# Kernel optimization log

Measured on AMD Instinct MI355X. Metric: run time of the kernel, lower is better.

Reference implementation:

```python
import jax, jax.numpy as jnp
import numpy as np

NUM_HEADS = 16
LN_EPS = 1e-5


def setup_inputs() -> dict:
    key = jax.random.key(0)
    k1, k2, k3 = jax.random.split(key, 3)
    E = 1024
    B, S = 4, 2048
    return {
        "rotation_params": jax.random.normal(k1, (E, E), dtype=jnp.float32) * (E ** -0.5),
        "entangle_params": jax.random.normal(k2, (E, E), dtype=jnp.float32) * (E ** -0.5),
        "inputs": jax.random.normal(k3, (B, S, E), dtype=jnp.float32),
        "ln_weight": jnp.ones((E,), dtype=jnp.float32),
        "ln_bias": jnp.zeros((E,), dtype=jnp.float32),
    }


def reference(rotation_params, entangle_params, inputs, ln_weight, ln_bias):
    x = inputs  # (B, S, E)
    B, S, E = x.shape
    H = NUM_HEADS
    D = E // H
    scale = D ** -0.5

    q = jnp.einsum('bse,ef->bsf', x, rotation_params)
    k = jnp.einsum('bse,ef->bsf', x, entangle_params)
    v = x  # forward uses raw inputs as values

    # split heads: (B, H, S, D)
    q = q.reshape(B, S, H, D).transpose(0, 2, 1, 3)
    k = k.reshape(B, S, H, D).transpose(0, 2, 1, 3)
    v = v.reshape(B, S, H, D).transpose(0, 2, 1, 3)

    scores = jnp.einsum('bhsd,bhtd->bhst', q, k) * scale  # (B, H, S, S)
    attn = jax.nn.softmax(scores, axis=-1)
    context = jnp.einsum('bhst,bhtd->bhsd', attn, v)
    context = context.transpose(0, 2, 1, 3).reshape(B, S, E)

    # residual + LayerNorm
    y = context + x
    mu = jnp.mean(y, axis=-1, keepdims=True)
    var = jnp.mean(jnp.square(y - mu), axis=-1, keepdims=True)
    y = (y - mu) * jax.lax.rsqrt(var + LN_EPS)
    return y * ln_weight + ln_bias
```

## Files before the change

kernel.cpp:

```cpp
#include <hip/hip_runtime.h>
#include <hip/hip_bf16.h>

#define LOG2E 1.44269504088896340736f

typedef __attribute__((ext_vector_type(8)))  short  short8;
typedef __attribute__((ext_vector_type(4)))  float  f32x4;
typedef __attribute__((ext_vector_type(16))) float  f32x16;

__device__ __forceinline__ unsigned short f2bf(float f) {
  unsigned u = __builtin_bit_cast(unsigned, f);
  return (unsigned short)((u + 0x8000u) >> 16);
}
__device__ __forceinline__ unsigned pkbf2(float a, float b) {
  unsigned A = __builtin_bit_cast(unsigned, a) + 0x8000u;
  unsigned B = __builtin_bit_cast(unsigned, b) + 0x8000u;
  return __builtin_amdgcn_perm(B, A, 0x07060302u);
}
__device__ __forceinline__ float hexp2(float x) {
  float r; asm("v_exp_f32 %0, %1" : "=v"(r) : "v"(x)); return r;
}
__device__ __forceinline__ void gl16(const void* g, void* l) {
  __builtin_amdgcn_global_load_lds(
      (const __attribute__((address_space(1))) void*)g,
      (__attribute__((address_space(3))) void*)l, 16, 0, 0);
}
__device__ __forceinline__ float vmax16(f32x16 s) {
  float a[8];
#pragma unroll
  for (int j = 0; j < 8; j++) a[j] = fmaxf(s[2 * j], s[2 * j + 1]);
#pragma unroll
  for (int j = 0; j < 4; j++) a[j] = fmaxf(a[j], a[j + 4]);
  return fmaxf(fmaxf(a[0], a[1]), fmaxf(a[2], a[3]));
}


__global__ __launch_bounds__(256) void prep_wt(const float* __restrict__ R,
                                               const float* __restrict__ En,
                                               unsigned short* __restrict__ Rt,
                                               unsigned short* __restrict__ Et) {
  const float* src = blockIdx.z ? En : R;
  unsigned short* dst = blockIdx.z ? Et : Rt;
  __shared__ unsigned short t[64][65];
  int e0 = blockIdx.y * 64, f0 = blockIdx.x * 64;
  int tid = threadIdx.x;
  int r = tid >> 2, c4 = (tid & 3) * 16;
#pragma unroll
  for (int j = 0; j < 16; j += 4) {
    float4 v = *(const float4*)(src + (size_t)(e0 + r) * 1024 + f0 + c4 + j);
    t[c4 + j + 0][r] = f2bf(v.x);
    t[c4 + j + 1][r] = f2bf(v.y);
    t[c4 + j + 2][r] = f2bf(v.z);
    t[c4 + j + 3][r] = f2bf(v.w);
  }
  __syncthreads();
  short8 o0, o1;
#pragma unroll
  for (int j = 0; j < 8; j++) {
    o0[j] = (short)t[r][c4 + j];
    o1[j] = (short)t[r][c4 + 8 + j];
  }
  *(short8*)(dst + (size_t)(f0 + r) * 1024 + e0 + c4) = o0;
  *(short8*)(dst + (size_t)(f0 + r) * 1024 + e0 + c4 + 8) = o1;
}

__global__ __launch_bounds__(256) void prep_vt(const float* __restrict__ x,
                                               unsigned short* __restrict__ vt,
                                               unsigned short* __restrict__ xb) {
  int bh = blockIdx.y, b = bh >> 4, h = bh & 15;
  int s0 = blockIdx.x * 64;
  __shared__ unsigned short t[64][65];
  int tid = threadIdx.x;
  int r = tid >> 2, c4 = (tid & 3) * 16;
#pragma unroll
  for (int j = 0; j < 16; j += 4) {
    float4 v = *(const float4*)(x + (size_t)(b * 2048 + s0 + r) * 1024 + h * 64 + c4 + j);
    ushort4 o;
    o.x = f2bf(v.x); o.y = f2bf(v.y); o.z = f2bf(v.z); o.w = f2bf(v.w);
    t[c4 + j + 0][r] = o.x;
    t[c4 + j + 1][r] = o.y;
    t[c4 + j + 2][r] = o.z;
    t[c4 + j + 3][r] = o.w;
    *(ushort4*)(xb + (size_t)(b * 2048 + s0 + r) * 1024 + h * 64 + c4 + j) = o;
  }
  __syncthreads();
  short8 o0, o1;
#pragma unroll
  for (int j = 0; j < 8; j++) {
    o0[j] = (short)t[r][c4 + j];
    o1[j] = (short)t[r][c4 + 8 + j];
  }
  *(short8*)(vt + (size_t)(bh * 64 + r) * 2048 + s0 + c4) = o0;
  *(short8*)(vt + (size_t)(bh * 64 + r) * 2048 + s0 + c4 + 8) = o1;
}

__global__ __launch_bounds__(256) void gemm_qk(const unsigned short* __restrict__ A,
                                               const unsigned short* __restrict__ Bw,
                                               unsigned short* __restrict__ out,
                                               float scale) {
  int m0 = blockIdx.x * 128, n0 = blockIdx.y * 128;
  int tid = threadIdx.x;
  int w = tid >> 6, l = tid & 63;
  int wr = w >> 1, wc = w & 1;
  int l15 = l & 15, lq = l >> 4;

  __shared__ unsigned short As[128 * 64];
  __shared__ unsigned short Bs[128 * 64];

  f32x4 acc[4][4] = {};

  for (int k0 = 0; k0 < 1024; k0 += 64) {
    __syncthreads();
#pragma unroll
    for (int i = 0; i < 4; i++) {
      int row = i * 32 + (tid >> 3), ch = tid & 7;
      gl16(A  + (size_t)(m0 + row) * 1024 + k0 + ((ch ^ (row & 7)) << 3),
           (char*)As + i * 4096 + w * 1024);
      gl16(Bw + (size_t)(n0 + row) * 1024 + k0 + ((ch ^ (row & 7)) << 3),
           (char*)Bs + i * 4096 + w * 1024);
    }
    __syncthreads();

    short8 af[4][2], bfr[4][2];
#pragma unroll
    for (int mf = 0; mf < 4; mf++)
#pragma unroll
      for (int kk = 0; kk < 2; kk++) {
        int row = wr * 64 + mf * 16 + l15;
        int kb2 = (kk * 32 + lq * 8) * 2;
        af[mf][kk] = *(const short8*)((const char*)As + row * 128 + (kb2 ^ ((row & 7) << 4)));
      }
#pragma unroll
    for (int nf = 0; nf < 4; nf++)
#pragma unroll
      for (int kk = 0; kk < 2; kk++) {
        int row = wc * 64 + nf * 16 + l15;
        int kb2 = (kk * 32 + lq * 8) * 2;
        bfr[nf][kk] = *(const short8*)((const char*)Bs + row * 128 + (kb2 ^ ((row & 7) << 4)));
      }
#pragma unroll
    for (int mf = 0; mf < 4; mf++)
#pragma unroll
      for (int nf = 0; nf < 4; nf++)
#pragma unroll
        for (int kk = 0; kk < 2; kk++)
          acc[mf][nf] = __builtin_amdgcn_mfma_f32_16x16x32_bf16(
              af[mf][kk], bfr[nf][kk], acc[mf][nf], 0, 0, 0);
  }

#pragma unroll
  for (int mf = 0; mf < 4; mf++)
#pragma unroll
    for (int nf = 0; nf < 4; nf++)
#pragma unroll
      for (int r = 0; r < 4; r++) {
        int grow = m0 + wr * 64 + mf * 16 + lq * 4 + r;
        int gcol = n0 + wc * 64 + nf * 16 + l15;
        out[(size_t)grow * 1024 + gcol] = f2bf(acc[mf][nf][r] * scale);
      }
}

__global__ __launch_bounds__(256) void attn_k(const unsigned short* __restrict__ Q,
                                              const unsigned short* __restrict__ K,
                                              const unsigned short* __restrict__ VT,
                                              float* __restrict__ ctx) {
  int f = blockIdx.x;
  int bh = ((f >> 7) << 3) | (f & 7);
  int qt = (f >> 3) & 15;
  int b = bh >> 4, h = bh & 15;
  int q0 = qt * 128;
  int tid = threadIdx.x;
  int w = tid >> 6, l = tid & 63;
  int lh = l >> 5, l31 = l & 31;

  __shared__ unsigned short Kl[2 * 64 * 64];
  __shared__ unsigned short Vl[2 * 64 * 64];

  int qrow = q0 + w * 32 + l31;
  const unsigned short* qp = Q + (size_t)(b * 2048 + qrow) * 1024 + h * 64;
  short8 qf[4];
#pragma unroll
  for (int dk = 0; dk < 4; dk++) qf[dk] = *(const short8*)(qp + dk * 16 + lh * 8);

  f32x16 cacc[2] = {};
  float mrun = -INFINITY, lsum = 0.f;

#define STAGE(buf, tt)                                                        \
  {                                                                           \
    _Pragma("unroll") for (int i_ = 0; i_ < 2; i_++) {                        \
      int row_ = i_ * 32 + (tid >> 3), ch_ = tid & 7;                         \
      gl16(K + (size_t)(b * 2048 + (tt) + row_) * 1024 + h * 64 +             \
               ((ch_ ^ (row_ & 7)) << 3),                                     \
           (char*)Kl + (buf) * 8192 + i_ * 4096 + w * 1024);                  \
      gl16(VT + (size_t)(bh * 64 + row_) * 2048 + (tt) +                      \
               ((ch_ ^ (row_ & 7)) << 3),                                     \
           (char*)Vl + (buf) * 8192 + i_ * 4096 + w * 1024);                  \
    }                                                                         \
  }

  STAGE(0, 0);
  __syncthreads();
  int cur = 0;

  for (int tc = 0; tc < 32; tc++) {
    int t0 = tc * 64;
    if (tc < 31) STAGE(cur ^ 1, t0 + 64);

    const char* Kb = (const char*)Kl + cur * 8192;
    const char* Vb = (const char*)Vl + cur * 8192;

    f32x16 sacc[2] = {};
    __builtin_amdgcn_s_setprio(1);
#pragma unroll
    for (int tf = 0; tf < 2; tf++) {
#pragma unroll
      for (int dk = 0; dk < 4; dk++) {
        int row = tf * 32 + l31;
        int kb2 = (dk * 16 + lh * 8) * 2;
        short8 kf = *(const short8*)(Kb + row * 128 + (kb2 ^ ((row & 7) << 4)));
        sacc[tf] = __builtin_amdgcn_mfma_f32_32x32x16_bf16(kf, qf[dk], sacc[tf], 0, 0, 0);
      }
    }
    __builtin_amdgcn_s_setprio(0);

    float tmax = fmaxf(vmax16(sacc[0]), vmax16(sacc[1]));
    {
      auto rr = __builtin_amdgcn_permlane32_swap(
          __builtin_bit_cast(unsigned, tmax), __builtin_bit_cast(unsigned, tmax), false, false);
      tmax = fmaxf(__builtin_bit_cast(float, rr[0]), __builtin_bit_cast(float, rr[1]));
    }

    if (!__all(tmax <= mrun + 8.f)) {
      float mnew = fmaxf(mrun, tmax);
      float alpha = hexp2(mrun - mnew);
      mrun = mnew;
      lsum *= alpha;
#pragma unroll
      for (int r = 0; r < 16; r++) {
        int rowq = (r & 3) + ((r >> 2) << 3) + (lh << 2);
        float ar = __shfl(alpha, rowq, 64);
        cacc[0][r] *= ar;
        cacc[1][r] *= ar;
      }
    }

    float racc0 = 0.f, racc1 = 0.f;
#pragma unroll
    for (int r = 0; r < 16; r++) {
      float p0 = hexp2(sacc[0][r] - mrun);
      float p1 = hexp2(sacc[1][r] - mrun);
      sacc[0][r] = p0;
      sacc[1][r] = p1;
      racc0 += p0;
      racc1 += p1;
    }
    float rs = racc0 + racc1;
    {
      auto rr = __builtin_amdgcn_permlane32_swap(
          __builtin_bit_cast(unsigned, rs), __builtin_bit_cast(unsigned, rs), false, false);
      rs = __builtin_bit_cast(float, rr[0]) + __builtin_bit_cast(float, rr[1]);
    }
    lsum += rs;

#pragma unroll
    for (int tf = 0; tf < 2; tf++) {
      short8 pa[2];
#pragma unroll
      for (int kk = 0; kk < 2; kk++) {
        int R = kk * 8;
        unsigned P0 = pkbf2(sacc[tf][R + 0], sacc[tf][R + 1]);
        unsigned P1 = pkbf2(sacc[tf][R + 2], sacc[tf][R + 3]);
        unsigned P2 = pkbf2(sacc[tf][R + 4], sacc[tf][R + 5]);
        unsigned P3 = pkbf2(sacc[tf][R + 6], sacc[tf][R + 7]);
        auto r02 = __builtin_amdgcn_permlane32_swap(P0, P2, false, false);
        auto r13 = __builtin_amdgcn_permlane32_swap(P1, P3, false, false);
        union { unsigned u[4]; short8 s8; } wv;
        wv.u[0] = r02[0];
        wv.u[1] = r13[0];
        wv.u[2] = r02[1];
        wv.u[3] = r13[1];
        pa[kk] = wv.s8;
      }
      __builtin_amdgcn_s_setprio(1);
#pragma unroll
      for (int kk = 0; kk < 2; kk++)
#pragma unroll
        for (int df = 0; df < 2; df++) {
          int drow = df * 32 + l31;
          int tb2 = (tf * 32 + kk * 16 + lh * 8) * 2;
          short8 vf = *(const short8*)(Vb + drow * 128 + (tb2 ^ ((l31 & 7) << 4)));
          cacc[df] = __builtin_amdgcn_mfma_f32_32x32x16_bf16(pa[kk], vf, cacc[df], 0, 0, 0);
        }
      __builtin_amdgcn_s_setprio(0);
    }

    __syncthreads();
    cur ^= 1;
  }
#undef STAGE

  float linv = 1.f / lsum;
#pragma unroll
  for (int r = 0; r < 16; r++) {
    int rowq = (r & 3) + ((r >> 2) << 3) + (lh << 2);
    float lr = __shfl(linv, rowq, 64);
    size_t base = (size_t)(b * 2048 + q0 + w * 32 + rowq) * 1024 + h * 64 + l31;
    ctx[base]      = cacc[0][r] * lr;
    ctx[base + 32] = cacc[1][r] * lr;
  }
}

__global__ __launch_bounds__(256) void ln_k(const float* __restrict__ ctx,
                                            const float* __restrict__ x,
                                            const float* __restrict__ wgt,
                                            const float* __restrict__ bgam,
                                            float* __restrict__ out) {
  int row = blockIdx.x;
  int tid = threadIdx.x;
  size_t base = (size_t)row * 1024 + tid * 4;
  float4 c = *(const float4*)(ctx + base);
  float4 xv = *(const float4*)(x + base);
  float4 y;
  y.x = c.x + xv.x; y.y = c.y + xv.y; y.z = c.z + xv.z; y.w = c.w + xv.w;
  float s  = y.x + y.y + y.z + y.w;
  float ss = y.x * y.x + y.y * y.y + y.z * y.z + y.w * y.w;
#pragma unroll
  for (int o = 32; o >= 1; o >>= 1) {
    s  += __shfl_xor(s, o, 64);
    ss += __shfl_xor(ss, o, 64);
  }
  __shared__ float sm[8];
  if ((tid & 63) == 0) { sm[(tid >> 6) * 2] = s; sm[(tid >> 6) * 2 + 1] = ss; }
  __syncthreads();
  s  = sm[0] + sm[2] + sm[4] + sm[6];
  ss = sm[1] + sm[3] + sm[5] + sm[7];
  float mu = s * (1.f / 1024.f);
  float var = ss * (1.f / 1024.f) - mu * mu;
  float rstd = rsqrtf(var + 1e-5f);
  float4 wv = *(const float4*)(wgt + tid * 4);
  float4 bv = *(const float4*)(bgam + tid * 4);
  float4 o4;
  o4.x = (y.x - mu) * rstd * wv.x + bv.x;
  o4.y = (y.y - mu) * rstd * wv.y + bv.y;
  o4.z = (y.z - mu) * rstd * wv.z + bv.z;
  o4.w = (y.w - mu) * rstd * wv.w + bv.w;
  *(float4*)(out + base) = o4;
}

extern "C" void kernel_launch(void* const* d_in, const int* in_sizes, int n_in,
                              void* d_out, int out_size, void* d_ws, size_t ws_size,
                              hipStream_t stream) {
  (void)in_sizes; (void)n_in; (void)out_size; (void)ws_size;
  const float* R  = (const float*)d_in[0];
  const float* En = (const float*)d_in[1];
  const float* x  = (const float*)d_in[2];
  const float* lw = (const float*)d_in[3];
  const float* lb = (const float*)d_in[4];
  float* out = (float*)d_out;

  char* ws = (char*)d_ws;
  unsigned short* xb  = (unsigned short*)(ws);
  unsigned short* qb  = (unsigned short*)(ws + (size_t)(16u << 20));
  unsigned short* kb  = (unsigned short*)(ws + (size_t)(32u << 20));
  unsigned short* vt  = (unsigned short*)(ws + (size_t)(48u << 20));
  float*          ctx = (float*)(ws + (size_t)(64u << 20));
  unsigned short* rt  = (unsigned short*)(ws + (size_t)(96u << 20));
  unsigned short* et  = (unsigned short*)(ws + (size_t)(98u << 20));

  prep_wt<<<dim3(16, 16, 2), 256, 0, stream>>>(R, En, rt, et);
  prep_vt<<<dim3(32, 64), 256, 0, stream>>>(x, vt, xb);
  gemm_qk<<<dim3(64, 8), 256, 0, stream>>>(xb, rt, qb, 0.125f * LOG2E);
  gemm_qk<<<dim3(64, 8), 256, 0, stream>>>(xb, et, kb, 1.0f);
  attn_k<<<1024, 256, 0, stream>>>(qb, kb, vt, ctx);
  ln_k<<<8192, 256, 0, stream>>>(ctx, x, lw, lb, out);
}
```

Measured before the change: 279.7 us.

## Fuse Q/K projections, unroll attention loop by two, store context in bf16

Merges the two projection GEMMs into one launch with a doubled N grid, relying on the transposed R and E weight buffers sitting next to each other in the workspace. The attention loop is unrolled by two with fixed LDS buffer offsets and precomputed swizzled addresses. Softmax now uses packed add and bf16 conversion instructions, and the row-sum cross-lane reduction moves out of the loop to run once at the end. The context is written as bf16 instead of fp32, halving the traffic between the attention and LayerNorm kernels at some precision cost, and launch bounds request higher occupancy.

```diff
diff --git a/kernel.cpp b/kernel.cpp
--- a/kernel.cpp
+++ b/kernel.cpp
@@ -4,6 +4,7 @@
 #define LOG2E 1.44269504088896340736f
 
 typedef __attribute__((ext_vector_type(8)))  short  short8;
+typedef __attribute__((ext_vector_type(2)))  float  f32x2;
 typedef __attribute__((ext_vector_type(4)))  float  f32x4;
 typedef __attribute__((ext_vector_type(16))) float  f32x16;
 
@@ -11,26 +12,25 @@
   unsigned u = __builtin_bit_cast(unsigned, f);
   return (unsigned short)((u + 0x8000u) >> 16);
 }
-__device__ __forceinline__ unsigned pkbf2(float a, float b) {
-  unsigned A = __builtin_bit_cast(unsigned, a) + 0x8000u;
-  unsigned B = __builtin_bit_cast(unsigned, b) + 0x8000u;
-  return __builtin_amdgcn_perm(B, A, 0x07060302u);
+__device__ __forceinline__ float bf2f(unsigned short u) {
+  return __builtin_bit_cast(float, (unsigned)u << 16);
+}
+__device__ __forceinline__ f32x2 pkadd(f32x2 a, f32x2 b) {
+  f32x2 r; asm("v_pk_add_f32 %0, %1, %2" : "=v"(r) : "v"(a), "v"(b)); return r;
+}
+__device__ __forceinline__ unsigned cvtpk2(float a, float b) {
+  unsigned r; asm("v_cvt_pk_bf16_f32 %0, %1, %2" : "=v"(r) : "v"(a), "v"(b)); return r;
 }
 __device__ __forceinline__ float hexp2(float x) {
   float r; asm("v_exp_f32 %0, %1" : "=v"(r) : "v"(x)); return r;
+}
+__device__ __forceinline__ float m3(float a, float b, float c) {
+  return fmaxf(fmaxf(a, b), c);
 }
 __device__ __forceinline__ void gl16(const void* g, void* l) {
   __builtin_amdgcn_global_load_lds(
       (const __attribute__((address_space(1))) void*)g,
       (__attribute__((address_space(3))) void*)l, 16, 0, 0);
-}
-__device__ __forceinline__ float vmax16(f32x16 s) {
-  float a[8];
-#pragma unroll
-  for (int j = 0; j < 8; j++) a[j] = fmaxf(s[2 * j], s[2 * j + 1]);
-#pragma unroll
-  for (int j = 0; j < 4; j++) a[j] = fmaxf(a[j], a[j + 4]);
-  return fmaxf(fmaxf(a[0], a[1]), fmaxf(a[2], a[3]));
 }
 
 
@@ -93,10 +93,11 @@
   *(short8*)(vt + (size_t)(bh * 64 + r) * 2048 + s0 + c4 + 8) = o1;
 }
 
-__global__ __launch_bounds__(256) void gemm_qk(const unsigned short* __restrict__ A,
-                                               const unsigned short* __restrict__ Bw,
-                                               unsigned short* __restrict__ out,
-                                               float scale) {
+__global__ __launch_bounds__(256) void gemm_qk2(const unsigned short* __restrict__ A,
+                                                const unsigned short* __restrict__ Bw,
+                                                unsigned short* __restrict__ qb,
+                                                unsigned short* __restrict__ kb,
+                                                float qs) {
   int m0 = blockIdx.x * 128, n0 = blockIdx.y * 128;
   int tid = threadIdx.x;
   int w = tid >> 6, l = tid & 63;
@@ -147,6 +148,9 @@
               af[mf][kk], bfr[nf][kk], acc[mf][nf], 0, 0, 0);
   }
 
+  unsigned short* out = (n0 < 1024) ? qb : kb;
+  float scale = (n0 < 1024) ? qs : 1.0f;
+  int cb = n0 & 1023;
 #pragma unroll
   for (int mf = 0; mf < 4; mf++)
 #pragma unroll
@@ -154,15 +158,15 @@
 #pragma unroll
       for (int r = 0; r < 4; r++) {
         int grow = m0 + wr * 64 + mf * 16 + lq * 4 + r;
-        int gcol = n0 + wc * 64 + nf * 16 + l15;
+        int gcol = cb + wc * 64 + nf * 16 + l15;
         out[(size_t)grow * 1024 + gcol] = f2bf(acc[mf][nf][r] * scale);
       }
 }
 
-__global__ __launch_bounds__(256) void attn_k(const unsigned short* __restrict__ Q,
-                                              const unsigned short* __restrict__ K,
-                                              const unsigned short* __restrict__ VT,
-                                              float* __restrict__ ctx) {
+__global__ __launch_bounds__(256, 4) void attn_k(const unsigned short* __restrict__ Q,
+                                                 const unsigned short* __restrict__ K,
+                                                 const unsigned short* __restrict__ VT,
+                                                 unsigned short* __restrict__ ctx) {
   int f = blockIdx.x;
   int bh = ((f >> 7) << 3) | (f & 7);
   int qt = (f >> 3) & 15;
@@ -181,8 +185,21 @@
 #pragma unroll
   for (int dk = 0; dk < 4; dk++) qf[dk] = *(const short8*)(qp + dk * 16 + lh * 8);
 
+  int key = (l31 & 7) << 4;
+  int koff[4], voff[4];
+#pragma unroll
+  for (int dk = 0; dk < 4; dk++) koff[dk] = l31 * 128 + ((dk * 32 + lh * 16) ^ key);
+#pragma unroll
+  for (int tf = 0; tf < 2; tf++)
+#pragma unroll
+    for (int kk = 0; kk < 2; kk++)
+      voff[tf * 2 + kk] = l31 * 128 + ((tf * 64 + kk * 32 + lh * 16) ^ key);
+
+  const char* KB = (const char*)Kl;
+  const char* VB = (const char*)Vl;
+
   f32x16 cacc[2] = {};
-  float mrun = -INFINITY, lsum = 0.f;
+  float mrun = -INFINITY, lsl = 0.f;
 
 #define STAGE(buf, tt)                                                        \
   {                                                                           \
@@ -197,119 +214,107 @@
     }                                                                         \
   }
 
+#define COMPUTE(IMM)                                                          \
+  do {                                                                        \
+    f32x16 sacc[2] = {};                                                      \
+    __builtin_amdgcn_s_setprio(1);                                            \
+    _Pragma("unroll") for (int tf = 0; tf < 2; tf++)                          \
+      _Pragma("unroll") for (int dk = 0; dk < 4; dk++) {                      \
+        short8 kf = *(const short8*)(KB + koff[dk] + (IMM) + tf * 4096);      \
+        sacc[tf] = __builtin_amdgcn_mfma_f32_32x32x16_bf16(kf, qf[dk],        \
+                                                           sacc[tf], 0, 0, 0);\
+      }                                                                       \
+    __builtin_amdgcn_s_setprio(0);                                            \
+    float t16[16];                                                            \
+    _Pragma("unroll") for (int j = 0; j < 16; j++)                            \
+      t16[j] = fmaxf(sacc[0][j], sacc[1][j]);                                 \
+    float t8[8];                                                              \
+    _Pragma("unroll") for (int j = 0; j < 8; j++)                             \
+      t8[j] = fmaxf(t16[j], t16[j + 8]);                                      \
+    float lmax = m3(m3(t8[0], t8[1], t8[2]), m3(t8[3], t8[4], t8[5]),         \
+                    fmaxf(t8[6], t8[7]));                                     \
+    if (!__all(lmax <= mrun + 8.f)) {                                         \
+      unsigned lu = __builtin_bit_cast(unsigned, lmax);                       \
+      auto rr = __builtin_amdgcn_permlane32_swap(lu, lu, false, false);       \
+      float pm = fmaxf(__builtin_bit_cast(float, rr[0]),                      \
+                       __builtin_bit_cast(float, rr[1]));                     \
+      float mnew = fmaxf(mrun, pm);                                           \
+      float alpha = hexp2(mrun - mnew);                                       \
+      mrun = mnew; lsl *= alpha;                                              \
+      _Pragma("unroll") for (int r = 0; r < 16; r++) {                        \
+        int rowq = (r & 3) + ((r >> 2) << 3) + (lh << 2);                     \
+        float ar = __shfl(alpha, rowq, 64);                                   \
+        cacc[0][r] *= ar; cacc[1][r] *= ar;                                   \
+      }                                                                       \
+    }                                                                         \
+    f32x2 negm2; negm2[0] = -mrun; negm2[1] = -mrun;                          \
+    f32x2 r2; r2[0] = 0.f; r2[1] = 0.f;                                       \
+    _Pragma("unroll") for (int tf = 0; tf < 2; tf++) {                        \
+      unsigned pw[8];                                                         \
+      _Pragma("unroll") for (int j = 0; j < 8; j++) {                         \
+        f32x2 s2; s2[0] = sacc[tf][2 * j]; s2[1] = sacc[tf][2 * j + 1];       \
+        f32x2 d = pkadd(s2, negm2);                                           \
+        float e0 = hexp2(d[0]), e1 = hexp2(d[1]);                             \
+        f32x2 e2; e2[0] = e0; e2[1] = e1;                                     \
+        r2 = pkadd(r2, e2);                                                   \
+        pw[j] = cvtpk2(e0, e1);                                               \
+      }                                                                       \
+      short8 pa[2];                                                           \
+      _Pragma("unroll") for (int kk = 0; kk < 2; kk++) {                      \
+        auto r02 = __builtin_amdgcn_permlane32_swap(pw[kk * 4 + 0],           \
+                                                    pw[kk * 4 + 2], false, false); \
+        auto r13 = __builtin_amdgcn_permlane32_swap(pw[kk * 4 + 1],           \
+                                                    pw[kk * 4 + 3], false, false); \
+        union { unsigned u[4]; short8 s8; } wv;                               \
+        wv.u[0] = r02[0]; wv.u[1] = r13[0];                                   \
+        wv.u[2] = r02[1]; wv.u[3] = r13[1];                                   \
+        pa[kk] = wv.s8;                                                       \
+      }                                                                       \
+      __builtin_amdgcn_s_setprio(1);                                          \
+      _Pragma("unroll") for (int kk = 0; kk < 2; kk++)                        \
+        _Pragma("unroll") for (int df = 0; df < 2; df++) {                    \
+          short8 vf = *(const short8*)(VB + voff[tf * 2 + kk] + (IMM) +       \
+                                       df * 4096);                            \
+          cacc[df] = __builtin_amdgcn_mfma_f32_32x32x16_bf16(pa[kk], vf,      \
+                                                             cacc[df], 0, 0, 0); \
+        }                                                                     \
+      __builtin_amdgcn_s_setprio(0);                                          \
+    }                                                                         \
+    lsl += r2[0] + r2[1];                                                     \
+  } while (0)
+
   STAGE(0, 0);
   __syncthreads();
-  int cur = 0;
-
-  for (int tc = 0; tc < 32; tc++) {
-    int t0 = tc * 64;
-    if (tc < 31) STAGE(cur ^ 1, t0 + 64);
-
-    const char* Kb = (const char*)Kl + cur * 8192;
-    const char* Vb = (const char*)Vl + cur * 8192;
-
-    f32x16 sacc[2] = {};
-    __builtin_amdgcn_s_setprio(1);
-#pragma unroll
-    for (int tf = 0; tf < 2; tf++) {
-#pragma unroll
-      for (int dk = 0; dk < 4; dk++) {
-        int row = tf * 32 + l31;
-        int kb2 = (dk * 16 + lh * 8) * 2;
-        short8 kf = *(const short8*)(Kb + row * 128 + (kb2 ^ ((row & 7) << 4)));
-        sacc[tf] = __builtin_amdgcn_mfma_f32_32x32x16_bf16(kf, qf[dk], sacc[tf], 0, 0, 0);
-      }
-    }
-    __builtin_amdgcn_s_setprio(0);
-
-    float tmax = fmaxf(vmax16(sacc[0]), vmax16(sacc[1]));
-    {
-      auto rr = __builtin_amdgcn_permlane32_swap(
-          __builtin_bit_cast(unsigned, tmax), __builtin_bit_cast(unsigned, tmax), false, false);
-      tmax = fmaxf(__builtin_bit_cast(float, rr[0]), __builtin_bit_cast(float, rr[1]));
-    }
-
-    if (!__all(tmax <= mrun + 8.f)) {
-      float mnew = fmaxf(mrun, tmax);
-      float alpha = hexp2(mrun - mnew);
-      mrun = mnew;
-      lsum *= alpha;
-#pragma unroll
-      for (int r = 0; r < 16; r++) {
-        int rowq = (r & 3) + ((r >> 2) << 3) + (lh << 2);
-        float ar = __shfl(alpha, rowq, 64);
-        cacc[0][r] *= ar;
-        cacc[1][r] *= ar;
-      }
-    }
-
-    float racc0 = 0.f, racc1 = 0.f;
-#pragma unroll
-    for (int r = 0; r < 16; r++) {
-      float p0 = hexp2(sacc[0][r] - mrun);
-      float p1 = hexp2(sacc[1][r] - mrun);
-      sacc[0][r] = p0;
-      sacc[1][r] = p1;
-      racc0 += p0;
-      racc1 += p1;
-    }
-    float rs = racc0 + racc1;
-    {
-      auto rr = __builtin_amdgcn_permlane32_swap(
-          __builtin_bit_cast(unsigned, rs), __builtin_bit_cast(unsigned, rs), false, false);
-      rs = __builtin_bit_cast(float, rr[0]) + __builtin_bit_cast(float, rr[1]);
-    }
-    lsum += rs;
-
-#pragma unroll
-    for (int tf = 0; tf < 2; tf++) {
-      short8 pa[2];
-#pragma unroll
-      for (int kk = 0; kk < 2; kk++) {
-        int R = kk * 8;
-        unsigned P0 = pkbf2(sacc[tf][R + 0], sacc[tf][R + 1]);
-        unsigned P1 = pkbf2(sacc[tf][R + 2], sacc[tf][R + 3]);
-        unsigned P2 = pkbf2(sacc[tf][R + 4], sacc[tf][R + 5]);
-        unsigned P3 = pkbf2(sacc[tf][R + 6], sacc[tf][R + 7]);
-        auto r02 = __builtin_amdgcn_permlane32_swap(P0, P2, false, false);
-        auto r13 = __builtin_amdgcn_permlane32_swap(P1, P3, false, false);
-        union { unsigned u[4]; short8 s8; } wv;
-        wv.u[0] = r02[0];
-        wv.u[1] = r13[0];
-        wv.u[2] = r02[1];
-        wv.u[3] = r13[1];
-        pa[kk] = wv.s8;
-      }
-      __builtin_amdgcn_s_setprio(1);
-#pragma unroll
-      for (int kk = 0; kk < 2; kk++)
-#pragma unroll
-        for (int df = 0; df < 2; df++) {
-          int drow = df * 32 + l31;
-          int tb2 = (tf * 32 + kk * 16 + lh * 8) * 2;
-          short8 vf = *(const short8*)(Vb + drow * 128 + (tb2 ^ ((l31 & 7) << 4)));
-          cacc[df] = __builtin_amdgcn_mfma_f32_32x32x16_bf16(pa[kk], vf, cacc[df], 0, 0, 0);
-        }
-      __builtin_amdgcn_s_setprio(0);
-    }
-
+
+  for (int tc2 = 0; tc2 < 16; tc2++) {
+    int t0 = tc2 * 128;
+    STAGE(1, t0 + 64);
+    COMPUTE(0);
     __syncthreads();
-    cur ^= 1;
+    if (tc2 < 15) STAGE(0, t0 + 128);
+    COMPUTE(8192);
+    __syncthreads();
   }
 #undef STAGE
-
-  float linv = 1.f / lsum;
+#undef COMPUTE
+
+  {
+    unsigned lu = __builtin_bit_cast(unsigned, lsl);
+    auto rr = __builtin_amdgcn_permlane32_swap(lu, lu, false, false);
+    lsl = __builtin_bit_cast(float, rr[0]) + __builtin_bit_cast(float, rr[1]);
+  }
+  float linv = 1.f / lsl;
 #pragma unroll
   for (int r = 0; r < 16; r++) {
     int rowq = (r & 3) + ((r >> 2) << 3) + (lh << 2);
     float lr = __shfl(linv, rowq, 64);
     size_t base = (size_t)(b * 2048 + q0 + w * 32 + rowq) * 1024 + h * 64 + l31;
-    ctx[base]      = cacc[0][r] * lr;
-    ctx[base + 32] = cacc[1][r] * lr;
-  }
-}
-
-__global__ __launch_bounds__(256) void ln_k(const float* __restrict__ ctx,
+    ctx[base]      = f2bf(cacc[0][r] * lr);
+    ctx[base + 32] = f2bf(cacc[1][r] * lr);
+  }
+}
+
+__global__ __launch_bounds__(256) void ln_k(const unsigned short* __restrict__ ctx,
                                             const float* __restrict__ x,
                                             const float* __restrict__ wgt,
                                             const float* __restrict__ bgam,
@@ -317,10 +322,11 @@
   int row = blockIdx.x;
   int tid = threadIdx.x;
   size_t base = (size_t)row * 1024 + tid * 4;
-  float4 c = *(const float4*)(ctx + base);
+  ushort4 cu = *(const ushort4*)(ctx + base);
   float4 xv = *(const float4*)(x + base);
   float4 y;
-  y.x = c.x + xv.x; y.y = c.y + xv.y; y.z = c.z + xv.z; y.w = c.w + xv.w;
+  y.x = bf2f(cu.x) + xv.x; y.y = bf2f(cu.y) + xv.y;
+  y.z = bf2f(cu.z) + xv.z; y.w = bf2f(cu.w) + xv.w;
   float s  = y.x + y.y + y.z + y.w;
   float ss = y.x * y.x + y.y * y.y + y.z * y.z + y.w * y.w;
 #pragma unroll
@@ -362,14 +368,13 @@
   unsigned short* qb  = (unsigned short*)(ws + (size_t)(16u << 20));
   unsigned short* kb  = (unsigned short*)(ws + (size_t)(32u << 20));
   unsigned short* vt  = (unsigned short*)(ws + (size_t)(48u << 20));
-  float*          ctx = (float*)(ws + (size_t)(64u << 20));
+  unsigned short* ctx = (unsigned short*)(ws + (size_t)(64u << 20));
   unsigned short* rt  = (unsigned short*)(ws + (size_t)(96u << 20));
   unsigned short* et  = (unsigned short*)(ws + (size_t)(98u << 20));
 
   prep_wt<<<dim3(16, 16, 2), 256, 0, stream>>>(R, En, rt, et);
   prep_vt<<<dim3(32, 64), 256, 0, stream>>>(x, vt, xb);
-  gemm_qk<<<dim3(64, 8), 256, 0, stream>>>(xb, rt, qb, 0.125f * LOG2E);
-  gemm_qk<<<dim3(64, 8), 256, 0, stream>>>(xb, et, kb, 1.0f);
+  gemm_qk2<<<dim3(64, 16), 256, 0, stream>>>(xb, rt, qb, kb, 0.125f * LOG2E);
   attn_k<<<1024, 256, 0, stream>>>(qb, kb, vt, ctx);
   ln_k<<<8192, 256, 0, stream>>>(ctx, x, lw, lb, out);
 }
```

Result: faster. 251.5 us (-10.1%).
